# Kernel tuning notes

Measured on AMD Instinct MI355X. Metric: run time of the kernel, lower is better.

## Reference

```python
import jax, jax.numpy as jnp
import numpy as np

N, F_IN, H1, H2, HEADS, E = 8192, 512, 128, 64, 3, 262144
NEG_SLOPE = 0.2  # PyG GATConv default negative_slope


def _add_self_loops(src, dst, n):
    loop = jnp.arange(n, dtype=src.dtype)
    return jnp.concatenate([src, loop]), jnp.concatenate([dst, loop])


def _gcn_conv(x, src, dst, W, b, n):
    # PyG GCNConv: h = x @ W, add self-loops, symmetric D^-1/2 A D^-1/2 aggregation, + bias
    h = x @ W
    s, d = _add_self_loops(src, dst, n)
    deg = jax.ops.segment_sum(jnp.ones(s.shape, h.dtype), d, num_segments=n)
    dinv = jnp.where(deg > 0, jax.lax.rsqrt(deg), 0.0)
    norm = dinv[s] * dinv[d]  # [E']
    return jax.ops.segment_sum(h[s] * norm[:, None], d, num_segments=n) + b


def _gat_conv(x, src, dst, W, a_src, a_dst, b, n, heads, concat):
    # PyG GATConv: per-head linear, LeakyReLU attention logits, segment softmax over
    # incoming edges per destination node, weighted scatter-aggregate.
    out_dim = W.shape[1] // heads
    h = (x @ W).reshape(n, heads, out_dim)  # [N, H, D]
    s, d = _add_self_loops(src, dst, n)
    a_s = jnp.einsum('nhd,hd->nh', h, a_src)
    a_d = jnp.einsum('nhd,hd->nh', h, a_dst)
    e = jax.nn.leaky_relu(a_s[s] + a_d[d], NEG_SLOPE)  # [E', H]
    m = jax.ops.segment_max(e, d, num_segments=n)      # stable softmax per dst segment
    ex = jnp.exp(e - m[d])
    den = jax.ops.segment_sum(ex, d, num_segments=n)
    msg = h[s] * (ex / den[d])[..., None]              # [E', H, D]
    out = jax.ops.segment_sum(msg, d, num_segments=n)  # [N, H, D]
    if concat:
        return out.reshape(n, heads * out_dim) + b
    return out.mean(axis=1) + b


def _forward(x, edge_index, gcn_W1, gcn_b1, gcn_Wmu, gcn_bmu, gcn_Wlv, gcn_blv,
             gat_W1, gat_as1, gat_ad1, gat_b1,
             gat_Wmu, gat_asmu, gat_admu, gat_bmu,
             gat_Wlv, gat_aslv, gat_adlv, gat_blv,
             eps_gcn, eps_gat):
    src, dst = edge_index[0], edge_index[1]
    n = x.shape[0]
    mu_g = lv_g = z_g = None
    for i in range(gcn_W1.shape[0]):  # gcn branches
        h = jax.nn.relu(_gcn_conv(x, src, dst, gcn_W1[i], gcn_b1[i], n))
        mu = _gcn_conv(h, src, dst, gcn_Wmu[i], gcn_bmu[i], n)
        lv = _gcn_conv(h, src, dst, gcn_Wlv[i], gcn_blv[i], n)
        z = mu + eps_gcn[i] * jnp.exp(lv)  # faithful: logvar passed as logstd
        mu_g = mu if mu_g is None else jnp.maximum(mu_g, mu)
        lv_g = lv if lv_g is None else jnp.maximum(lv_g, lv)
        z_g = z if z_g is None else jnp.maximum(z_g, z)
    mu_a = lv_a = z_a = None
    for i in range(gat_W1.shape[0]):  # gat branches
        h = jax.nn.relu(_gat_conv(x, src, dst, gat_W1[i], gat_as1[i], gat_ad1[i], gat_b1[i], n, HEADS, True))
        mu = _gat_conv(h, src, dst, gat_Wmu[i], gat_asmu[i], gat_admu[i], gat_bmu[i], n, HEADS, False)
        lv = _gat_conv(h, src, dst, gat_Wlv[i], gat_aslv[i], gat_adlv[i], gat_blv[i], n, HEADS, False)
        z = mu + eps_gat[i] * jnp.exp(lv)
        mu_a = mu if mu_a is None else jnp.maximum(mu_a, mu)
        lv_a = lv if lv_a is None else jnp.maximum(lv_a, lv)
        z_a = z if z_a is None else jnp.maximum(z_a, z)
    mu_max = jnp.maximum(mu_g, mu_a)
    lv_max = jnp.maximum(lv_g, lv_a)
    z_max = jnp.maximum(z_g, z_a)
    adj = jax.nn.sigmoid(z_max @ z_max.T)  # InnerProductDecoder.forward_all(sigmoid=True)
    return adj, mu_max, lv_max


def setup_inputs():
    key = jax.random.key(0)
    ki = iter(jax.random.split(key, 32))
    p = lambda shape: jax.random.normal(next(ki), shape, dtype=jnp.float32) * 0.05
    x = jax.random.normal(next(ki), (N, F_IN), dtype=jnp.float32)
    edge_index = jax.random.randint(next(ki), (2, E), 0, N)
    return dict(
        x=x, edge_index=edge_index,
        gcn_W1=p((2, F_IN, H1)), gcn_b1=p((2, H1)),
        gcn_Wmu=p((2, H1, H2)), gcn_bmu=p((2, H2)),
        gcn_Wlv=p((2, H1, H2)), gcn_blv=p((2, H2)),
        gat_W1=p((2, F_IN, HEADS * H1)), gat_as1=p((2, HEADS, H1)),
        gat_ad1=p((2, HEADS, H1)), gat_b1=p((2, HEADS * H1)),
        gat_Wmu=p((2, HEADS * H1, HEADS * H2)), gat_asmu=p((2, HEADS, H2)),
        gat_admu=p((2, HEADS, H2)), gat_bmu=p((2, H2)),
        gat_Wlv=p((2, HEADS * H1, HEADS * H2)), gat_aslv=p((2, HEADS, H2)),
        gat_adlv=p((2, HEADS, H2)), gat_blv=p((2, H2)),
        eps_gcn=jax.random.normal(next(ki), (2, N, H2), dtype=jnp.float32),
        eps_gat=jax.random.normal(next(ki), (2, N, H2), dtype=jnp.float32),
    )


def reference(x, edge_index, gcn_W1, gcn_b1, gcn_Wmu, gcn_bmu, gcn_Wlv, gcn_blv,
              gat_W1, gat_as1, gat_ad1, gat_b1,
              gat_Wmu, gat_asmu, gat_admu, gat_bmu,
              gat_Wlv, gat_aslv, gat_adlv, gat_blv,
              eps_gcn, eps_gat):
    return _forward(x, edge_index, gcn_W1, gcn_b1, gcn_Wmu, gcn_bmu, gcn_Wlv, gcn_blv,
                    gat_W1, gat_as1, gat_ad1, gat_b1,
                    gat_Wmu, gat_asmu, gat_admu, gat_bmu,
                    gat_Wlv, gat_aslv, gat_adlv, gat_blv,
                    eps_gcn, eps_gat)
```

## Files before the change

### kernel.cpp

```cpp
#include <hip/hip_runtime.h>
#include <hip/hip_bf16.h>
#include <math.h>
#include <stddef.h>

#define NN 8192
#define NEG_SLOPE 0.2f

typedef _Float16 h8 __attribute__((ext_vector_type(8)));
typedef __attribute__((ext_vector_type(4))) float f32x4;

__device__ __forceinline__ float lrelu(float x) { return x > 0.f ? x : NEG_SLOPE * x; }
__device__ __forceinline__ float sigf(float x) { return 1.f / (1.f + __expf(-x)); }

__device__ __forceinline__ unsigned short f16b(float x) {
    _Float16 h = (_Float16)x;
    unsigned short u;
    __builtin_memcpy(&u, &h, 2);
    return u;
}
__device__ __forceinline__ float f16f(unsigned short u) {
    _Float16 h;
    __builtin_memcpy(&h, &u, 2);
    return (float)h;
}
__device__ __forceinline__ void splith(float x, unsigned short& hu, unsigned short& lu) {
    _Float16 h = (_Float16)x;
    float hf = (float)h;
    _Float16 l = (_Float16)(x - hf);
    __builtin_memcpy(&hu, &h, 2);
    __builtin_memcpy(&lu, &l, 2);
}
__device__ __forceinline__ float2 unpkh(unsigned int v) {
    float2 r;
    r.x = f16f((unsigned short)(v & 0xffffu));
    r.y = f16f((unsigned short)(v >> 16));
    return r;
}
__device__ __forceinline__ unsigned int packh(float a, float b) {
    return (unsigned int)f16b(a) | ((unsigned int)f16b(b) << 16);
}
__device__ __forceinline__ void acc8(float* a, uint4 v, float w) {
    float2 p;
    p = unpkh(v.x); a[0] += w * p.x; a[1] += w * p.y;
    p = unpkh(v.y); a[2] += w * p.x; a[3] += w * p.y;
    p = unpkh(v.z); a[4] += w * p.x; a[5] += w * p.y;
    p = unpkh(v.w); a[6] += w * p.x; a[7] += w * p.y;
}

__device__ __forceinline__ void gll16(const unsigned short* g, unsigned short* l) {
    __builtin_amdgcn_global_load_lds(
        (const __attribute__((address_space(1))) unsigned int*)g,
        (__attribute__((address_space(3))) unsigned int*)l, 16, 0, 0);
}

__global__ void k_zero(int* __restrict__ p, int n) {
    int i = blockIdx.x * blockDim.x + threadIdx.x;
    if (i < n) p[i] = 0;
}
__global__ void k_count(const int* __restrict__ dst, int* __restrict__ cnt, int E) {
    int i = blockIdx.x * blockDim.x + threadIdx.x;
    if (i < E) atomicAdd(&cnt[dst[i]], 1);
}
__global__ void k_dinv(const int* __restrict__ cnt, float* __restrict__ dinv) {
    int i = blockIdx.x * blockDim.x + threadIdx.x;
    if (i < NN) dinv[i] = rsqrtf((float)(cnt[i] + 1));
}
__global__ void k_scan(const int* __restrict__ cnt, int* __restrict__ row_ptr) {
    __shared__ int part[1024];
    int t = threadIdx.x;
    int base = t * 8;
    int loc[8];
    int s = 0;
    #pragma unroll
    for (int j = 0; j < 8; ++j) { loc[j] = s; s += cnt[base + j]; }
    part[t] = s;
    __syncthreads();
    for (int off = 1; off < 1024; off <<= 1) {
        int v = (t >= off) ? part[t - off] : 0;
        __syncthreads();
        part[t] += v;
        __syncthreads();
    }
    int pre = (t == 0) ? 0 : part[t - 1];
    #pragma unroll
    for (int j = 0; j < 8; ++j) row_ptr[base + j] = pre + loc[j];
    if (t == 1023) row_ptr[NN] = part[1023];
}
__global__ void k_fill(const int* __restrict__ src, const int* __restrict__ dst,
                       const int* __restrict__ row_ptr, int* __restrict__ cursor,
                       int* __restrict__ csr_src, int E) {
    int i = blockIdx.x * blockDim.x + threadIdx.x;
    if (i < E) {
        int d = dst[i];
        csr_src[row_ptr[d] + atomicAdd(&cursor[d], 1)] = src[i];
    }
}

__global__ void k_cvt_x(const float* __restrict__ x, unsigned short* __restrict__ xh) {
    int i = blockIdx.x * 256 + threadIdx.x;
    int m = i >> 7, k4 = (i & 127) * 4;
    float4 v = *(const float4*)(x + (size_t)m * 512 + k4);
    ushort4 o;
    o.x = f16b(v.x); o.y = f16b(v.y); o.z = f16b(v.z); o.w = f16b(v.w);
    *(ushort4*)&xh[(size_t)m * 512 + k4] = o;
}

__global__ void k_wT(const float* __restrict__ W, unsigned short* __restrict__ Wt,
                     int K, int N, size_t wt_z_stride, int noff, int noff_z) {
    int b = blockIdx.z;
    W += (size_t)b * K * N;
    Wt += (size_t)b * wt_z_stride;
    int rowbase = noff + b * noff_z;
    int k0 = blockIdx.x * 32, n0 = blockIdx.y * 32;
    __shared__ float tl[32][33];
    int tid = threadIdx.x;
    int r = tid >> 5, cc = tid & 31;
    #pragma unroll
    for (int c = 0; c < 4; ++c)
        tl[r + c * 8][cc] = W[(size_t)(k0 + r + c * 8) * N + n0 + cc];
    __syncthreads();
    #pragma unroll
    for (int c = 0; c < 4; ++c) {
        int n = r + c * 8, k = cc;
        Wt[(size_t)(rowbase + n0 + n) * K + k0 + k] = f16b(tl[k][n]);
    }
}

template <int ROWS>
__device__ __forceinline__ void stage(const unsigned short* __restrict__ gbase, int lda,
                                      unsigned short* lds, int wid, int lane) {
    #pragma unroll
    for (int c = 0; c < ROWS / 32; ++c) {
        int chunk = c * 4 + wid;
        int row = chunk * 8 + (lane >> 3);
        int g = (lane & 7) ^ (row & 7);
        gll16(gbase + (size_t)row * lda + g * 8, lds + chunk * 512);
    }
}
__device__ __forceinline__ h8 fragrh(const unsigned short* lds, int row, int kg) {
    return *(const h8*)(lds + row * 64 + ((kg ^ (row & 7)) * 8));
}

template <int TERMS, int EPI>
__global__ __launch_bounds__(256) void k_gemm2(
    const unsigned short* __restrict__ A2, size_t azs, int lda,
    const unsigned short* __restrict__ B2, size_t bzs, int ldb,
    void* __restrict__ Cv, size_t czs, int ldc, int K) {
    __shared__ __align__(16) unsigned short sAh[128 * 64];
    __shared__ __align__(16) unsigned short sBh[64 * 64];
    __shared__ __align__(16) unsigned short sAl[(TERMS == 3) ? 128 * 64 : 8];
    __shared__ __align__(16) unsigned short sBl[(TERMS == 3) ? 64 * 64 : 8];
    const int tid = threadIdx.x;
    const int wid = tid >> 6, lane = tid & 63;
    const int wr = wid >> 1, wc = wid & 1;
    const int lr = lane & 15, lg = lane >> 4;
    const int m0 = blockIdx.x * 128, n0 = blockIdx.y * 64;
    const int z = blockIdx.z;
    A2 += (size_t)z * azs;
    B2 += (size_t)z * bzs;

    const f32x4 zero4 = {0.f, 0.f, 0.f, 0.f};
    f32x4 acc[4][2];
    #pragma unroll
    for (int m = 0; m < 4; ++m)
        #pragma unroll
        for (int n = 0; n < 2; ++n) acc[m][n] = zero4;

    for (int k0 = 0; k0 < K; k0 += 64) {
        stage<128>(A2 + (size_t)m0 * lda + k0, lda, sAh, wid, lane);
        stage<64> (B2 + (size_t)n0 * ldb + k0, ldb, sBh, wid, lane);
        if (TERMS == 3) {
            stage<128>(A2 + (size_t)m0 * lda + K + k0, lda, sAl, wid, lane);
            stage<64> (B2 + (size_t)n0 * ldb + K + k0, ldb, sBl, wid, lane);
        }
        __syncthreads();
        #pragma unroll
        for (int ks = 0; ks < 2; ++ks) {
            const int kg = ks * 4 + lg;
            h8 ah[4], al[4], bh[2], bl[2];
            #pragma unroll
            for (int m = 0; m < 4; ++m) {
                int row = wr * 64 + m * 16 + lr;
                ah[m] = fragrh(sAh, row, kg);
                if (TERMS == 3) al[m] = fragrh(sAl, row, kg);
            }
            #pragma unroll
            for (int n = 0; n < 2; ++n) {
                int row = wc * 32 + n * 16 + lr;
                bh[n] = fragrh(sBh, row, kg);
                if (TERMS == 3) bl[n] = fragrh(sBl, row, kg);
            }
            #pragma unroll
            for (int m = 0; m < 4; ++m)
                #pragma unroll
                for (int n = 0; n < 2; ++n) {
                    acc[m][n] = __builtin_amdgcn_mfma_f32_16x16x32_f16(ah[m], bh[n], acc[m][n], 0, 0, 0);
                    if (TERMS == 3) {
                        acc[m][n] = __builtin_amdgcn_mfma_f32_16x16x32_f16(al[m], bh[n], acc[m][n], 0, 0, 0);
                        acc[m][n] = __builtin_amdgcn_mfma_f32_16x16x32_f16(ah[m], bl[n], acc[m][n], 0, 0, 0);
                    }
                }
        }
        __syncthreads();
    }
    #pragma unroll
    for (int m = 0; m < 4; ++m)
        #pragma unroll
        for (int n = 0; n < 2; ++n)
            #pragma unroll
            for (int j = 0; j < 4; ++j) {
                int row = m0 + wr * 64 + m * 16 + lg * 4 + j;
                int col = n0 + wc * 32 + n * 16 + lr;
                float o = acc[m][n][j];
                if (EPI == 1) {
                    ((float*)Cv + (size_t)z * czs)[(size_t)row * ldc + col] = sigf(o);
                } else if (EPI == 2) {
                    ((unsigned short*)Cv + (size_t)z * czs)[(size_t)row * ldc + col] = f16b(o);
                } else {
                    ((float*)Cv + (size_t)z * czs)[(size_t)row * ldc + col] = o;
                }
            }
}

template <int RELU_BIAS>
__global__ void k_gcn_agg(const uint4* __restrict__ v4, const float* __restrict__ dinv,
                          const int* __restrict__ rp, const int* __restrict__ cs,
                          const float* __restrict__ b1, unsigned int* __restrict__ outu) {
    int d = blockIdx.x;
    int t = threadIdx.x;
    int g = t >> 5, lr = t & 31;
    float dd = dinv[d];
    float a[8] = {0.f, 0.f, 0.f, 0.f, 0.f, 0.f, 0.f, 0.f};
    if (g == 0) {
        uint4 sv = v4[(size_t)d * 32 + lr];
        acc8(a, sv, dd);
    }
    int e0 = rp[d], e1 = rp[d + 1];
    int j = e0 + g;
    for (; j + 8 < e1; j += 16) {
        int s0 = cs[j], s1 = cs[j + 8];
        float w0 = dinv[s0], w1 = dinv[s1];
        uint4 v0 = v4[(size_t)s0 * 32 + lr];
        uint4 v1 = v4[(size_t)s1 * 32 + lr];
        acc8(a, v0, w0);
        acc8(a, v1, w1);
    }
    if (j < e1) {
        int s = cs[j];
        uint4 v = v4[(size_t)s * 32 + lr];
        acc8(a, v, dinv[s]);
    }
    __shared__ float red[8][256];
    #pragma unroll
    for (int i = 0; i < 8; ++i) red[g][lr * 8 + i] = a[i];
    __syncthreads();
    if (t < 128) {
        int c0 = 2 * t, c1 = 2 * t + 1;
        float s0 = 0.f, s1 = 0.f;
        #pragma unroll
        for (int gg = 0; gg < 8; ++gg) { s0 += red[gg][c0]; s1 += red[gg][c1]; }
        float o0, o1;
        if (RELU_BIAS) {
            o0 = fmaxf(dd * s0 + b1[c0], 0.f);
            o1 = fmaxf(dd * s1 + b1[c1], 0.f);
        } else {
            o0 = dd * s0;
            o1 = dd * s1;
        }
        outu[(size_t)d * 128 + t] = packh(o0, o1);
    }
}

__global__ void k_gat_log1(const unsigned int* __restrict__ xwu, const float* __restrict__ a_s,
                           const float* __restrict__ a_d, float* __restrict__ as_n,
                           float* __restrict__ ad_n) {
    int br = blockIdx.z;
    int n = blockIdx.x;
    int hd = threadIdx.x >> 6, lane = threadIdx.x & 63;
    const unsigned int* hp = xwu + (size_t)n * 384 + br * 192 + hd * 64;
    const float* av = a_s + br * 384 + hd * 128;
    const float* dv = a_d + br * 384 + hd * 128;
    float2 f = unpkh(hp[lane]);
    float ss = f.x * av[2 * lane] + f.y * av[2 * lane + 1];
    float sd = f.x * dv[2 * lane] + f.y * dv[2 * lane + 1];
    #pragma unroll
    for (int off = 32; off; off >>= 1) {
        ss += __shfl_down(ss, off);
        sd += __shfl_down(sd, off);
    }
    if (lane == 0) {
        as_n[(size_t)br * NN * 3 + n * 3 + hd] = ss;
        ad_n[(size_t)br * NN * 3 + n * 3 + hd] = sd;
    }
}

__global__ void k_gat_log2(const unsigned short* __restrict__ h2gb, const float* __restrict__ asmu,
                           const float* __restrict__ aslv, const float* __restrict__ admu,
                           const float* __restrict__ adlv, float* __restrict__ as_n,
                           float* __restrict__ ad_n) {
    int zz = blockIdx.z;
    int br = zz >> 1, mt = zz & 1;
    int n = blockIdx.x;
    int hd = threadIdx.x >> 6, lane = threadIdx.x & 63;
    const unsigned short* hp = h2gb + (size_t)br * NN * 384 + (size_t)n * 384 + mt * 192 + hd * 64;
    const float* av = (mt ? aslv : asmu) + br * 192 + hd * 64;
    const float* dv = (mt ? adlv : admu) + br * 192 + hd * 64;
    float hv = f16f(hp[lane]);
    float ss = hv * av[lane];
    float sd = hv * dv[lane];
    #pragma unroll
    for (int off = 32; off; off >>= 1) {
        ss += __shfl_down(ss, off);
        sd += __shfl_down(sd, off);
    }
    if (lane == 0) {
        as_n[(size_t)zz * NN * 3 + n * 3 + hd] = ss;
        ad_n[(size_t)zz * NN * 3 + n * 3 + hd] = sd;
    }
}

__global__ void k_gat_attn(const float* __restrict__ as_n, const float* __restrict__ ad_n,
                           const int* __restrict__ rp, const int* __restrict__ cs,
                           float* __restrict__ w_csr, float* __restrict__ w_self, int E3) {
    int zz = blockIdx.z;
    as_n += (size_t)zz * NN * 3;
    ad_n += (size_t)zz * NN * 3;
    w_csr += (size_t)zz * E3;
    w_self += (size_t)zz * NN * 3;
    int d = blockIdx.x;
    int hd = threadIdx.x >> 6, lane = threadIdx.x & 63;
    int e0 = rp[d], e1 = rp[d + 1];
    float add = ad_n[d * 3 + hd];
    float eself = lrelu(as_n[d * 3 + hd] + add);
    float mx = eself;
    for (int j = e0 + lane; j < e1; j += 64) {
        float e = lrelu(as_n[cs[j] * 3 + hd] + add);
        w_csr[(size_t)j * 3 + hd] = e;
        mx = fmaxf(mx, e);
    }
    #pragma unroll
    for (int off = 32; off; off >>= 1) mx = fmaxf(mx, __shfl_xor(mx, off));
    float sm = (lane == 0) ? __expf(eself - mx) : 0.f;
    for (int j = e0 + lane; j < e1; j += 64)
        sm += __expf(w_csr[(size_t)j * 3 + hd] - mx);
    #pragma unroll
    for (int off = 32; off; off >>= 1) sm += __shfl_xor(sm, off);
    float inv = 1.f / sm;
    if (lane == 0) w_self[d * 3 + hd] = __expf(eself - mx) * inv;
    for (int j = e0 + lane; j < e1; j += 64)
        w_csr[(size_t)j * 3 + hd] = __expf(w_csr[(size_t)j * 3 + hd] - mx) * inv;
}

__global__ void k_gat_agg1(const uint4* __restrict__ xw4, const float* __restrict__ w_csr,
                           const float* __restrict__ w_self, const int* __restrict__ rp,
                           const int* __restrict__ cs, const float* __restrict__ b1,
                           unsigned int* __restrict__ h1su, int E3) {
    int d = blockIdx.x;
    int t = threadIdx.x;
    int g = t / 96, lr = t - g * 96;
    int c = lr * 8;
    int br = c >= 384 ? 1 : 0;
    int cb = c - br * 384;
    int hd = cb >> 7;
    const float* wc = w_csr + (size_t)br * E3;
    float a[8] = {0.f, 0.f, 0.f, 0.f, 0.f, 0.f, 0.f, 0.f};
    if (g == 0) {
        float ws = w_self[(size_t)br * NN * 3 + d * 3 + hd];
        uint4 sv = xw4[(size_t)d * 96 + lr];
        acc8(a, sv, ws);
    }
    int e0 = rp[d], e1 = rp[d + 1];
    int j = e0 + g;
    for (; j + 4 < e1; j += 8) {
        int s0 = cs[j], s1 = cs[j + 4];
        float w0 = wc[(size_t)j * 3 + hd];
        float w1 = wc[(size_t)(j + 4) * 3 + hd];
        uint4 v0 = xw4[(size_t)s0 * 96 + lr];
        uint4 v1 = xw4[(size_t)s1 * 96 + lr];
        acc8(a, v0, w0);
        acc8(a, v1, w1);
    }
    if (j < e1) {
        int s = cs[j];
        float w = wc[(size_t)j * 3 + hd];
        uint4 v = xw4[(size_t)s * 96 + lr];
        acc8(a, v, w);
    }
    __shared__ float red[4][768];
    #pragma unroll
    for (int i = 0; i < 8; ++i) red[g][c + i] = a[i];
    __syncthreads();
    {
        int c0 = 2 * t, c1 = 2 * t + 1;
        float s0 = 0.f, s1 = 0.f;
        #pragma unroll
        for (int gg = 0; gg < 4; ++gg) { s0 += red[gg][c0]; s1 += red[gg][c1]; }
        float o0 = fmaxf(s0 + b1[c0], 0.f);
        float o1 = fmaxf(s1 + b1[c1], 0.f);
        h1su[(size_t)d * 384 + t] = packh(o0, o1);
    }
}

__global__ void k_gat_agg2(const uint4* __restrict__ h2g4, const float* __restrict__ w_csr,
                           const float* __restrict__ w_self, const int* __restrict__ rp,
                           const int* __restrict__ cs, const float* __restrict__ bmu,
                           const float* __restrict__ blv, float* __restrict__ mt_gat, int E3) {
    int d = blockIdx.x;
    int t = threadIdx.x;
    int g = t / 96, lr = t - g * 96;
    int br = lr / 48, li = lr - br * 48;
    int c = li * 8;
    int mt = c >= 192 ? 1 : 0;
    int cm = c - mt * 192;
    int hd = cm >> 6;
    const float* wc = w_csr + (size_t)(br * 2 + mt) * E3;
    const uint4* hp = h2g4 + (size_t)br * NN * 48;
    float a[8] = {0.f, 0.f, 0.f, 0.f, 0.f, 0.f, 0.f, 0.f};
    if (g == 0) {
        float ws = w_self[(size_t)(br * 2 + mt) * NN * 3 + d * 3 + hd];
        uint4 sv = hp[(size_t)d * 48 + li];
        acc8(a, sv, ws);
    }
    int e0 = rp[d], e1 = rp[d + 1];
    int j = e0 + g;
    for (; j + 4 < e1; j += 8) {
        int s0 = cs[j], s1 = cs[j + 4];
        float w0 = wc[(size_t)j * 3 + hd];
        float w1 = wc[(size_t)(j + 4) * 3 + hd];
        uint4 v0 = hp[(size_t)s0 * 48 + li];
        uint4 v1 = hp[(size_t)s1 * 48 + li];
        acc8(a, v0, w0);
        acc8(a, v1, w1);
    }
    if (j < e1) {
        int s = cs[j];
        float w = wc[(size_t)j * 3 + hd];
        uint4 v = hp[(size_t)s * 48 + li];
        acc8(a, v, w);
    }
    __shared__ float red[4][768];
    #pragma unroll
    for (int i = 0; i < 8; ++i) red[g][br * 384 + c + i] = a[i];
    __syncthreads();
    if (t < 256) {
        int obr = t >> 7, omt = (t >> 6) & 1, dd2 = t & 63;
        int base = obr * 384 + omt * 192;
        float tot = 0.f;
        #pragma unroll
        for (int gg = 0; gg < 4; ++gg)
            tot += red[gg][base + dd2] + red[gg][base + 64 + dd2] + red[gg][base + 128 + dd2];
        const float* bias = omt ? blv : bmu;
        float v = tot * (1.f / 3.f) + bias[obr * 64 + dd2];
        mt_gat[((size_t)(obr * 2 + omt) * NN + d) * 64 + dd2] = v;
    }
}

__global__ void k_finalize(const float* __restrict__ muv_gcn, const float* __restrict__ gcn_bmu,
                           const float* __restrict__ gcn_blv, const float* __restrict__ mt_gat,
                           const float* __restrict__ eps_gcn, const float* __restrict__ eps_gat,
                           float* __restrict__ mu_o, float* __restrict__ lv_o,
                           unsigned short* __restrict__ z2) {
    int i = blockIdx.x * 256 + threadIdx.x;
    int d = i >> 6, c = i & 63;
    const size_t NN64 = (size_t)NN * 64;
    float mu, lv, zm;
    {
        float m = muv_gcn[(size_t)d * 128 + c] + gcn_bmu[c];
        float l = muv_gcn[(size_t)d * 128 + 64 + c] + gcn_blv[c];
        float z = m + eps_gcn[i] * __expf(l);
        mu = m; lv = l; zm = z;
    }
    {
        float m = muv_gcn[NN64 * 2 + (size_t)d * 128 + c] + gcn_bmu[64 + c];
        float l = muv_gcn[NN64 * 2 + (size_t)d * 128 + 64 + c] + gcn_blv[64 + c];
        float z = m + eps_gcn[NN64 + i] * __expf(l);
        mu = fmaxf(mu, m); lv = fmaxf(lv, l); zm = fmaxf(zm, z);
    }
    #pragma unroll
    for (int br = 0; br < 2; ++br) {
        float m = mt_gat[(size_t)(br * 2 + 0) * NN64 + i];
        float l = mt_gat[(size_t)(br * 2 + 1) * NN64 + i];
        float z = m + eps_gat[(size_t)br * NN64 + i] * __expf(l);
        mu = fmaxf(mu, m); lv = fmaxf(lv, l); zm = fmaxf(zm, z);
    }
    mu_o[i] = mu;
    lv_o[i] = lv;
    unsigned short hh, ll;
    splith(zm, hh, ll);
    z2[(size_t)d * 128 + c] = hh;
    z2[(size_t)d * 128 + 64 + c] = ll;
}

extern "C" void kernel_launch(void* const* d_in, const int* in_sizes, int n_in,
                              void* d_out, int out_size, void* d_ws, size_t ws_size,
                              hipStream_t stream) {
    const float* x  = (const float*)d_in[0];
    const int*   ei = (const int*)d_in[1];
    const int E = in_sizes[1] / 2;
    const int E3 = E * 3;
    const int* src = ei;
    const int* dst = ei + E;

    const float* gcn_W1  = (const float*)d_in[2];
    const float* gcn_b1  = (const float*)d_in[3];
    const float* gcn_Wmu = (const float*)d_in[4];
    const float* gcn_bmu = (const float*)d_in[5];
    const float* gcn_Wlv = (const float*)d_in[6];
    const float* gcn_blv = (const float*)d_in[7];
    const float* gat_W1  = (const float*)d_in[8];
    const float* gat_as1 = (const float*)d_in[9];
    const float* gat_ad1 = (const float*)d_in[10];
    const float* gat_b1  = (const float*)d_in[11];
    const float* gat_Wmu = (const float*)d_in[12];
    const float* gat_asmu= (const float*)d_in[13];
    const float* gat_admu= (const float*)d_in[14];
    const float* gat_bmu = (const float*)d_in[15];
    const float* gat_Wlv = (const float*)d_in[16];
    const float* gat_aslv= (const float*)d_in[17];
    const float* gat_adlv= (const float*)d_in[18];
    const float* gat_blv = (const float*)d_in[19];
    const float* eps_gcn = (const float*)d_in[20];
    const float* eps_gat = (const float*)d_in[21];

    char* p = (char*)d_ws;
    auto alloc = [&](size_t bytes) {
        void* r = (void*)p;
        p += (bytes + 255) & ~(size_t)255;
        return r;
    };
    int*   cnt     = (int*)alloc((size_t)NN * 4);
    int*   cursor  = (int*)alloc((size_t)NN * 4);
    int*   row_ptr = (int*)alloc((size_t)(NN + 1) * 4);
    int*   csr_src = (int*)alloc((size_t)E * 4);
    float* dinv    = (float*)alloc((size_t)NN * 4);
    float* as_n1   = (float*)alloc((size_t)2 * NN * 3 * 4);
    float* ad_n1   = (float*)alloc((size_t)2 * NN * 3 * 4);
    float* wself1  = (float*)alloc((size_t)2 * NN * 3 * 4);
    float* wcsr1   = (float*)alloc((size_t)2 * E3 * 4);
    float* as_n2   = (float*)alloc((size_t)4 * NN * 3 * 4);
    float* ad_n2   = (float*)alloc((size_t)4 * NN * 3 * 4);
    float* wself2  = (float*)alloc((size_t)4 * NN * 3 * 4);
    float* wcsr2   = (float*)alloc((size_t)4 * E3 * 4);
    unsigned short* x2h      = (unsigned short*)alloc((size_t)NN * 512 * 2);
    unsigned short* wt_gcn1  = (unsigned short*)alloc((size_t)256 * 512 * 2);
    unsigned short* wt_gcnmuv= (unsigned short*)alloc((size_t)2 * 128 * 128 * 2);
    unsigned short* wt_gat1  = (unsigned short*)alloc((size_t)768 * 512 * 2);
    unsigned short* wt_gatmuv= (unsigned short*)alloc((size_t)2 * 384 * 384 * 2);
    unsigned short* xwb  = (unsigned short*)alloc((size_t)NN * 768 * 2);
    unsigned short* hb   = (unsigned short*)alloc((size_t)NN * 256 * 2);
    unsigned short* hA   = (unsigned short*)alloc((size_t)NN * 256 * 2);
    float* muv_gcn = (float*)alloc((size_t)2 * NN * 128 * 4);
    unsigned short* h1s  = (unsigned short*)alloc((size_t)NN * 768 * 2);
    unsigned short* h2gb = (unsigned short*)alloc((size_t)2 * NN * 384 * 2);
    float* mt_gat  = (float*)alloc((size_t)4 * NN * 64 * 4);
    unsigned short* z2 = (unsigned short*)alloc((size_t)NN * 128 * 2);

    float* adj  = (float*)d_out;
    float* mu_o = adj + (size_t)NN * NN;
    float* lv_o = mu_o + (size_t)NN * 64;

    k_zero<<<(2 * NN + 255) / 256, 256, 0, stream>>>(cnt, 2 * NN);
    k_count<<<(E + 255) / 256, 256, 0, stream>>>(dst, cnt, E);
    k_dinv<<<(NN + 255) / 256, 256, 0, stream>>>(cnt, dinv);
    k_scan<<<1, 1024, 0, stream>>>(cnt, row_ptr);
    k_fill<<<(E + 255) / 256, 256, 0, stream>>>(src, dst, row_ptr, cursor, csr_src, E);

    k_cvt_x<<<NN * 512 / 4 / 256, 256, 0, stream>>>(x, x2h);
    k_wT<<<dim3(16, 4, 2), 256, 0, stream>>>(gcn_W1, wt_gcn1, 512, 128, 0, 0, 128);
    k_wT<<<dim3(4, 2, 2), 256, 0, stream>>>(gcn_Wmu, wt_gcnmuv, 128, 64, (size_t)128 * 128, 0, 0);
    k_wT<<<dim3(4, 2, 2), 256, 0, stream>>>(gcn_Wlv, wt_gcnmuv, 128, 64, (size_t)128 * 128, 64, 0);
    k_wT<<<dim3(16, 12, 2), 256, 0, stream>>>(gat_W1, wt_gat1, 512, 384, 0, 0, 384);
    k_wT<<<dim3(12, 6, 2), 256, 0, stream>>>(gat_Wmu, wt_gatmuv, 384, 192, (size_t)384 * 384, 0, 0);
    k_wT<<<dim3(12, 6, 2), 256, 0, stream>>>(gat_Wlv, wt_gatmuv, 384, 192, (size_t)384 * 384, 192, 0);

    k_gemm2<1, 2><<<dim3(64, 4, 1), 256, 0, stream>>>(x2h, 0, 512, wt_gcn1, 0, 512,
                                                      xwb, 0, 256, 512);
    k_gcn_agg<1><<<NN, 256, 0, stream>>>((const uint4*)xwb, dinv, row_ptr, csr_src,
                                         gcn_b1, (unsigned int*)hb);
    k_gcn_agg<0><<<NN, 256, 0, stream>>>((const uint4*)hb, dinv, row_ptr, csr_src,
                                         nullptr, (unsigned int*)hA);
    k_gemm2<1, 0><<<dim3(64, 2, 2), 256, 0, stream>>>(hA, 128, 256, wt_gcnmuv,
                                                      (size_t)128 * 128, 128,
                                                      muv_gcn, (size_t)NN * 128, 128, 128);

    k_gemm2<1, 2><<<dim3(64, 12, 1), 256, 0, stream>>>(x2h, 0, 512, wt_gat1, 0, 512,
                                                       xwb, 0, 768, 512);
    k_gat_log1<<<dim3(NN, 1, 2), 192, 0, stream>>>((const unsigned int*)xwb, gat_as1,
                                                   gat_ad1, as_n1, ad_n1);
    k_gat_attn<<<dim3(NN, 1, 2), 192, 0, stream>>>(as_n1, ad_n1, row_ptr, csr_src,
                                                   wcsr1, wself1, E3);
    k_gat_agg1<<<NN, 384, 0, stream>>>((const uint4*)xwb, wcsr1, wself1, row_ptr, csr_src,
                                       gat_b1, (unsigned int*)h1s, E3);
    k_gemm2<1, 2><<<dim3(64, 6, 2), 256, 0, stream>>>(h1s, 384, 768, wt_gatmuv,
                                                      (size_t)384 * 384, 384,
                                                      h2gb, (size_t)NN * 384, 384, 384);
    k_gat_log2<<<dim3(NN, 1, 4), 192, 0, stream>>>(h2gb, gat_asmu, gat_aslv, gat_admu,
                                                   gat_adlv, as_n2, ad_n2);
    k_gat_attn<<<dim3(NN, 1, 4), 192, 0, stream>>>(as_n2, ad_n2, row_ptr, csr_src,
                                                   wcsr2, wself2, E3);
    k_gat_agg2<<<NN, 384, 0, stream>>>((const uint4*)h2gb, wcsr2, wself2, row_ptr, csr_src,
                                       gat_bmu, gat_blv, mt_gat, E3);

    k_finalize<<<NN * 64 / 256, 256, 0, stream>>>(muv_gcn, gcn_bmu, gcn_blv, mt_gat,
                                                  eps_gcn, eps_gat, mu_o, lv_o, z2);
    k_gemm2<3, 1><<<dim3(64, 128, 1), 256, 0, stream>>>(z2, 0, 128, z2, 0, 128,
                                                        adj, 0, NN, 64);
}
```

Baseline: 376.1 us.

## Split graph aggregation kernels across feature slices with head-major attention weights

The GCN and GAT aggregation kernels now launch a second grid dimension, so each block handles one feature slice (a branch or head) of a destination node instead of the whole row. Neighbour indices, and for GCN the normalisation weights, are staged once in shared memory. Attention weights are stored head-major so that reads along consecutive edges are contiguous. The final sigmoid adjacency output uses nontemporal stores to limit cache pollution from the large N×N write. In exchange, each slice block re-reads the CSR indices, and there are more, smaller blocks to schedule.

```diff
diff --git a/kernel.cpp b/kernel.cpp
--- a/kernel.cpp
+++ b/kernel.cpp
@@ -213,7 +213,8 @@
                 int col = n0 + wc * 32 + n * 16 + lr;
                 float o = acc[m][n][j];
                 if (EPI == 1) {
-                    ((float*)Cv + (size_t)z * czs)[(size_t)row * ldc + col] = sigf(o);
+                    float* cp = (float*)Cv + (size_t)z * czs + (size_t)row * ldc + col;
+                    __builtin_nontemporal_store(sigf(o), cp);
                 } else if (EPI == 2) {
                     ((unsigned short*)Cv + (size_t)z * czs)[(size_t)row * ldc + col] = f16b(o);
                 } else {
@@ -223,51 +224,49 @@
 }
 
 template <int RELU_BIAS>
-__global__ void k_gcn_agg(const uint4* __restrict__ v4, const float* __restrict__ dinv,
-                          const int* __restrict__ rp, const int* __restrict__ cs,
-                          const float* __restrict__ b1, unsigned int* __restrict__ outu) {
+__global__ __launch_bounds__(256) void k_gcn_agg(
+    const uint4* __restrict__ v4, const float* __restrict__ dinv,
+    const int* __restrict__ rp, const int* __restrict__ cs,
+    const float* __restrict__ b1, unsigned int* __restrict__ outu) {
     int d = blockIdx.x;
+    int sl = blockIdx.y;
     int t = threadIdx.x;
-    int g = t >> 5, lr = t & 31;
+    int g = t >> 4, lr = t & 15;
     float dd = dinv[d];
+    const uint4* vb = v4 + sl * 16;
     float a[8] = {0.f, 0.f, 0.f, 0.f, 0.f, 0.f, 0.f, 0.f};
-    if (g == 0) {
-        uint4 sv = v4[(size_t)d * 32 + lr];
-        acc8(a, sv, dd);
-    }
+    if (g == 0) acc8(a, vb[(size_t)d * 32 + lr], dd);
     int e0 = rp[d], e1 = rp[d + 1];
-    int j = e0 + g;
-    for (; j + 8 < e1; j += 16) {
-        int s0 = cs[j], s1 = cs[j + 8];
-        float w0 = dinv[s0], w1 = dinv[s1];
-        uint4 v0 = v4[(size_t)s0 * 32 + lr];
-        uint4 v1 = v4[(size_t)s1 * 32 + lr];
-        acc8(a, v0, w0);
-        acc8(a, v1, w1);
-    }
-    if (j < e1) {
-        int s = cs[j];
-        uint4 v = v4[(size_t)s * 32 + lr];
-        acc8(a, v, dinv[s]);
-    }
-    __shared__ float red[8][256];
+    int deg = e1 - e0;
+    int dcap = deg < 512 ? deg : 512;
+    __shared__ int se[512];
+    __shared__ float sw[512];
+    for (int q = t; q < dcap; q += 256) { int s = cs[e0 + q]; se[q] = s; sw[q] = dinv[s]; }
+    __syncthreads();
+    for (int q = g; q < dcap; q += 16)
+        acc8(a, vb[(size_t)se[q] * 32 + lr], sw[q]);
+    for (int q = dcap + g; q < deg; q += 16) {
+        int s = cs[e0 + q];
+        acc8(a, vb[(size_t)s * 32 + lr], dinv[s]);
+    }
+    __shared__ float red[16][128];
     #pragma unroll
     for (int i = 0; i < 8; ++i) red[g][lr * 8 + i] = a[i];
     __syncthreads();
-    if (t < 128) {
-        int c0 = 2 * t, c1 = 2 * t + 1;
+    if (t < 64) {
+        int c0 = 2 * t, c1 = c0 + 1;
         float s0 = 0.f, s1 = 0.f;
         #pragma unroll
-        for (int gg = 0; gg < 8; ++gg) { s0 += red[gg][c0]; s1 += red[gg][c1]; }
+        for (int gg = 0; gg < 16; ++gg) { s0 += red[gg][c0]; s1 += red[gg][c1]; }
         float o0, o1;
         if (RELU_BIAS) {
-            o0 = fmaxf(dd * s0 + b1[c0], 0.f);
-            o1 = fmaxf(dd * s1 + b1[c1], 0.f);
+            o0 = fmaxf(dd * s0 + b1[sl * 128 + c0], 0.f);
+            o1 = fmaxf(dd * s1 + b1[sl * 128 + c1], 0.f);
         } else {
             o0 = dd * s0;
             o1 = dd * s1;
         }
-        outu[(size_t)d * 128 + t] = packh(o0, o1);
+        outu[(size_t)d * 128 + sl * 64 + t] = packh(o0, o1);
     }
 }
 
@@ -321,137 +320,113 @@
 
 __global__ void k_gat_attn(const float* __restrict__ as_n, const float* __restrict__ ad_n,
                            const int* __restrict__ rp, const int* __restrict__ cs,
-                           float* __restrict__ w_csr, float* __restrict__ w_self, int E3) {
+                           float* __restrict__ w_csr, float* __restrict__ w_self, int E) {
     int zz = blockIdx.z;
     as_n += (size_t)zz * NN * 3;
     ad_n += (size_t)zz * NN * 3;
-    w_csr += (size_t)zz * E3;
     w_self += (size_t)zz * NN * 3;
     int d = blockIdx.x;
     int hd = threadIdx.x >> 6, lane = threadIdx.x & 63;
+    float* wh = w_csr + ((size_t)zz * 3 + hd) * E;
     int e0 = rp[d], e1 = rp[d + 1];
     float add = ad_n[d * 3 + hd];
     float eself = lrelu(as_n[d * 3 + hd] + add);
     float mx = eself;
     for (int j = e0 + lane; j < e1; j += 64) {
         float e = lrelu(as_n[cs[j] * 3 + hd] + add);
-        w_csr[(size_t)j * 3 + hd] = e;
+        wh[j] = e;
         mx = fmaxf(mx, e);
     }
     #pragma unroll
     for (int off = 32; off; off >>= 1) mx = fmaxf(mx, __shfl_xor(mx, off));
     float sm = (lane == 0) ? __expf(eself - mx) : 0.f;
     for (int j = e0 + lane; j < e1; j += 64)
-        sm += __expf(w_csr[(size_t)j * 3 + hd] - mx);
+        sm += __expf(wh[j] - mx);
     #pragma unroll
     for (int off = 32; off; off >>= 1) sm += __shfl_xor(sm, off);
     float inv = 1.f / sm;
     if (lane == 0) w_self[d * 3 + hd] = __expf(eself - mx) * inv;
     for (int j = e0 + lane; j < e1; j += 64)
-        w_csr[(size_t)j * 3 + hd] = __expf(w_csr[(size_t)j * 3 + hd] - mx) * inv;
-}
-
-__global__ void k_gat_agg1(const uint4* __restrict__ xw4, const float* __restrict__ w_csr,
-                           const float* __restrict__ w_self, const int* __restrict__ rp,
-                           const int* __restrict__ cs, const float* __restrict__ b1,
-                           unsigned int* __restrict__ h1su, int E3) {
+        wh[j] = __expf(wh[j] - mx) * inv;
+}
+
+__global__ __launch_bounds__(256) void k_gat_agg1(
+    const uint4* __restrict__ xw4, const float* __restrict__ w_h,
+    const float* __restrict__ w_self, const int* __restrict__ rp,
+    const int* __restrict__ cs, const float* __restrict__ b1,
+    unsigned int* __restrict__ h1su, int E) {
     int d = blockIdx.x;
+    int sl = blockIdx.y;
+    int br = sl / 3, hd = sl - br * 3;
     int t = threadIdx.x;
-    int g = t / 96, lr = t - g * 96;
-    int c = lr * 8;
-    int br = c >= 384 ? 1 : 0;
-    int cb = c - br * 384;
-    int hd = cb >> 7;
-    const float* wc = w_csr + (size_t)br * E3;
+    int g = t >> 4, lr = t & 15;
+    const uint4* vb = xw4 + br * 48 + hd * 16;
+    const float* wc = w_h + (size_t)sl * E;
     float a[8] = {0.f, 0.f, 0.f, 0.f, 0.f, 0.f, 0.f, 0.f};
-    if (g == 0) {
-        float ws = w_self[(size_t)br * NN * 3 + d * 3 + hd];
-        uint4 sv = xw4[(size_t)d * 96 + lr];
-        acc8(a, sv, ws);
-    }
+    if (g == 0) acc8(a, vb[(size_t)d * 96 + lr], w_self[(size_t)br * NN * 3 + d * 3 + hd]);
     int e0 = rp[d], e1 = rp[d + 1];
-    int j = e0 + g;
-    for (; j + 4 < e1; j += 8) {
-        int s0 = cs[j], s1 = cs[j + 4];
-        float w0 = wc[(size_t)j * 3 + hd];
-        float w1 = wc[(size_t)(j + 4) * 3 + hd];
-        uint4 v0 = xw4[(size_t)s0 * 96 + lr];
-        uint4 v1 = xw4[(size_t)s1 * 96 + lr];
-        acc8(a, v0, w0);
-        acc8(a, v1, w1);
-    }
-    if (j < e1) {
-        int s = cs[j];
-        float w = wc[(size_t)j * 3 + hd];
-        uint4 v = xw4[(size_t)s * 96 + lr];
-        acc8(a, v, w);
-    }
-    __shared__ float red[4][768];
-    #pragma unroll
-    for (int i = 0; i < 8; ++i) red[g][c + i] = a[i];
-    __syncthreads();
-    {
-        int c0 = 2 * t, c1 = 2 * t + 1;
+    int deg = e1 - e0;
+    int dcap = deg < 512 ? deg : 512;
+    __shared__ int se[512];
+    for (int q = t; q < dcap; q += 256) se[q] = cs[e0 + q];
+    __syncthreads();
+    for (int q = g; q < dcap; q += 16)
+        acc8(a, vb[(size_t)se[q] * 96 + lr], wc[e0 + q]);
+    for (int q = dcap + g; q < deg; q += 16)
+        acc8(a, vb[(size_t)cs[e0 + q] * 96 + lr], wc[e0 + q]);
+    __shared__ float red[16][128];
+    #pragma unroll
+    for (int i = 0; i < 8; ++i) red[g][lr * 8 + i] = a[i];
+    __syncthreads();
+    if (t < 64) {
+        int c0 = 2 * t, c1 = c0 + 1;
         float s0 = 0.f, s1 = 0.f;
         #pragma unroll
-        for (int gg = 0; gg < 4; ++gg) { s0 += red[gg][c0]; s1 += red[gg][c1]; }
-        float o0 = fmaxf(s0 + b1[c0], 0.f);
-        float o1 = fmaxf(s1 + b1[c1], 0.f);
-        h1su[(size_t)d * 384 + t] = packh(o0, o1);
-    }
-}
-
-__global__ void k_gat_agg2(const uint4* __restrict__ h2g4, const float* __restrict__ w_csr,
-                           const float* __restrict__ w_self, const int* __restrict__ rp,
-                           const int* __restrict__ cs, const float* __restrict__ bmu,
-                           const float* __restrict__ blv, float* __restrict__ mt_gat, int E3) {
+        for (int gg = 0; gg < 16; ++gg) { s0 += red[gg][c0]; s1 += red[gg][c1]; }
+        int cb = br * 384 + hd * 128;
+        float o0 = fmaxf(s0 + b1[cb + c0], 0.f);
+        float o1 = fmaxf(s1 + b1[cb + c1], 0.f);
+        h1su[(size_t)d * 384 + br * 192 + hd * 64 + t] = packh(o0, o1);
+    }
+}
+
+__global__ __launch_bounds__(192) void k_gat_agg2(
+    const uint4* __restrict__ h2g4, const float* __restrict__ w_h,
+    const float* __restrict__ w_self, const int* __restrict__ rp,
+    const int* __restrict__ cs, const float* __restrict__ bmu,
+    const float* __restrict__ blv, float* __restrict__ mt_gat, int E) {
     int d = blockIdx.x;
+    int sl = blockIdx.y;
+    int br = sl >> 1, mt = sl & 1;
     int t = threadIdx.x;
-    int g = t / 96, lr = t - g * 96;
-    int br = lr / 48, li = lr - br * 48;
-    int c = li * 8;
-    int mt = c >= 192 ? 1 : 0;
-    int cm = c - mt * 192;
-    int hd = cm >> 6;
-    const float* wc = w_csr + (size_t)(br * 2 + mt) * E3;
-    const uint4* hp = h2g4 + (size_t)br * NN * 48;
+    int g = t / 24, lr = t - g * 24;
+    int hd = lr >> 3;
+    const uint4* vb = h2g4 + (size_t)br * NN * 48 + mt * 24;
+    const float* wc = w_h + ((size_t)sl * 3 + hd) * E;
     float a[8] = {0.f, 0.f, 0.f, 0.f, 0.f, 0.f, 0.f, 0.f};
-    if (g == 0) {
-        float ws = w_self[(size_t)(br * 2 + mt) * NN * 3 + d * 3 + hd];
-        uint4 sv = hp[(size_t)d * 48 + li];
-        acc8(a, sv, ws);
-    }
+    if (g == 0) acc8(a, vb[(size_t)d * 48 + lr], w_self[(size_t)sl * NN * 3 + d * 3 + hd]);
     int e0 = rp[d], e1 = rp[d + 1];
-    int j = e0 + g;
-    for (; j + 4 < e1; j += 8) {
-        int s0 = cs[j], s1 = cs[j + 4];
-        float w0 = wc[(size_t)j * 3 + hd];
-        float w1 = wc[(size_t)(j + 4) * 3 + hd];
-        uint4 v0 = hp[(size_t)s0 * 48 + li];
-        uint4 v1 = hp[(size_t)s1 * 48 + li];
-        acc8(a, v0, w0);
-        acc8(a, v1, w1);
-    }
-    if (j < e1) {
-        int s = cs[j];
-        float w = wc[(size_t)j * 3 + hd];
-        uint4 v = hp[(size_t)s * 48 + li];
-        acc8(a, v, w);
-    }
-    __shared__ float red[4][768];
-    #pragma unroll
-    for (int i = 0; i < 8; ++i) red[g][br * 384 + c + i] = a[i];
-    __syncthreads();
-    if (t < 256) {
-        int obr = t >> 7, omt = (t >> 6) & 1, dd2 = t & 63;
-        int base = obr * 384 + omt * 192;
+    int deg = e1 - e0;
+    int dcap = deg < 512 ? deg : 512;
+    __shared__ int se[512];
+    for (int q = t; q < dcap; q += 192) se[q] = cs[e0 + q];
+    __syncthreads();
+    for (int q = g; q < dcap; q += 8)
+        acc8(a, vb[(size_t)se[q] * 48 + lr], wc[e0 + q]);
+    for (int q = dcap + g; q < deg; q += 8)
+        acc8(a, vb[(size_t)cs[e0 + q] * 48 + lr], wc[e0 + q]);
+    __shared__ float red[8][192];
+    #pragma unroll
+    for (int i = 0; i < 8; ++i) red[g][lr * 8 + i] = a[i];
+    __syncthreads();
+    if (t < 64) {
         float tot = 0.f;
         #pragma unroll
-        for (int gg = 0; gg < 4; ++gg)
-            tot += red[gg][base + dd2] + red[gg][base + 64 + dd2] + red[gg][base + 128 + dd2];
-        const float* bias = omt ? blv : bmu;
-        float v = tot * (1.f / 3.f) + bias[obr * 64 + dd2];
-        mt_gat[((size_t)(obr * 2 + omt) * NN + d) * 64 + dd2] = v;
+        for (int gg = 0; gg < 8; ++gg)
+            tot += red[gg][t] + red[gg][64 + t] + red[gg][128 + t];
+        const float* bias = mt ? blv : bmu;
+        float o = tot * (1.f / 3.f) + bias[br * 64 + t];
+        mt_gat[((size_t)sl * NN + d) * 64 + t] = o;
     }
 }
 
@@ -497,7 +472,6 @@
     const float* x  = (const float*)d_in[0];
     const int*   ei = (const int*)d_in[1];
     const int E = in_sizes[1] / 2;
-    const int E3 = E * 3;
     const int* src = ei;
     const int* dst = ei + E;
 
@@ -536,11 +510,11 @@
     float* as_n1   = (float*)alloc((size_t)2 * NN * 3 * 4);
     float* ad_n1   = (float*)alloc((size_t)2 * NN * 3 * 4);
     float* wself1  = (float*)alloc((size_t)2 * NN * 3 * 4);
-    float* wcsr1   = (float*)alloc((size_t)2 * E3 * 4);
+    float* wcsr1   = (float*)alloc((size_t)2 * 3 * E * 4);
     float* as_n2   = (float*)alloc((size_t)4 * NN * 3 * 4);
     float* ad_n2   = (float*)alloc((size_t)4 * NN * 3 * 4);
     float* wself2  = (float*)alloc((size_t)4 * NN * 3 * 4);
-    float* wcsr2   = (float*)alloc((size_t)4 * E3 * 4);
+    float* wcsr2   = (float*)alloc((size_t)4 * 3 * E * 4);
     unsigned short* x2h      = (unsigned short*)alloc((size_t)NN * 512 * 2);
     unsigned short* wt_gcn1  = (unsigned short*)alloc((size_t)256 * 512 * 2);
     unsigned short* wt_gcnmuv= (unsigned short*)alloc((size_t)2 * 128 * 128 * 2);
@@ -575,10 +549,10 @@
 
     k_gemm2<1, 2><<<dim3(64, 4, 1), 256, 0, stream>>>(x2h, 0, 512, wt_gcn1, 0, 512,
                                                       xwb, 0, 256, 512);
-    k_gcn_agg<1><<<NN, 256, 0, stream>>>((const uint4*)xwb, dinv, row_ptr, csr_src,
-                                         gcn_b1, (unsigned int*)hb);
-    k_gcn_agg<0><<<NN, 256, 0, stream>>>((const uint4*)hb, dinv, row_ptr, csr_src,
-                                         nullptr, (unsigned int*)hA);
+    k_gcn_agg<1><<<dim3(NN, 2), 256, 0, stream>>>((const uint4*)xwb, dinv, row_ptr, csr_src,
+                                                  gcn_b1, (unsigned int*)hb);
+    k_gcn_agg<0><<<dim3(NN, 2), 256, 0, stream>>>((const uint4*)hb, dinv, row_ptr, csr_src,
+                                                  nullptr, (unsigned int*)hA);
     k_gemm2<1, 0><<<dim3(64, 2, 2), 256, 0, stream>>>(hA, 128, 256, wt_gcnmuv,
                                                       (size_t)128 * 128, 128,
                                                       muv_gcn, (size_t)NN * 128, 128, 128);
@@ -588,18 +562,18 @@
     k_gat_log1<<<dim3(NN, 1, 2), 192, 0, stream>>>((const unsigned int*)xwb, gat_as1,
                                                    gat_ad1, as_n1, ad_n1);
     k_gat_attn<<<dim3(NN, 1, 2), 192, 0, stream>>>(as_n1, ad_n1, row_ptr, csr_src,
-                                                   wcsr1, wself1, E3);
-    k_gat_agg1<<<NN, 384, 0, stream>>>((const uint4*)xwb, wcsr1, wself1, row_ptr, csr_src,
-                                       gat_b1, (unsigned int*)h1s, E3);
+                                                   wcsr1, wself1, E);
+    k_gat_agg1<<<dim3(NN, 6), 256, 0, stream>>>((const uint4*)xwb, wcsr1, wself1, row_ptr,
+                                                csr_src, gat_b1, (unsigned int*)h1s, E);
     k_gemm2<1, 2><<<dim3(64, 6, 2), 256, 0, stream>>>(h1s, 384, 768, wt_gatmuv,
                                                       (size_t)384 * 384, 384,
                                                       h2gb, (size_t)NN * 384, 384, 384);
     k_gat_log2<<<dim3(NN, 1, 4), 192, 0, stream>>>(h2gb, gat_asmu, gat_aslv, gat_admu,
                                                    gat_adlv, as_n2, ad_n2);
     k_gat_attn<<<dim3(NN, 1, 4), 192, 0, stream>>>(as_n2, ad_n2, row_ptr, csr_src,
-                                                   wcsr2, wself2, E3);
-    k_gat_agg2<<<NN, 384, 0, stream>>>((const uint4*)h2gb, wcsr2, wself2, row_ptr, csr_src,
-                                       gat_bmu, gat_blv, mt_gat, E3);
+                                                   wcsr2, wself2, E);
+    k_gat_agg2<<<dim3(NN, 4), 192, 0, stream>>>((const uint4*)h2gb, wcsr2, wself2, row_ptr,
+                                                csr_src, gat_bmu, gat_blv, mt_gat, E);
 
     k_finalize<<<NN * 64 / 256, 256, 0, stream>>>(muv_gcn, gcn_bmu, gcn_blv, mt_gat,
                                                   eps_gcn, eps_gat, mu_o, lv_o, z2);
```

Measured after the change: 422.4 us. 12.3% more time.
